# Kernel tuning notes

Hardware: AMD Instinct MI355X
Metric: run time of the kernel (lower is better)

Reference implementation:

```python
import jax, jax.numpy as jnp
import numpy as np

B, T, E, H = 8, 1024, 1024, 16
D = E // H  # per-head dim = 64


def setup_inputs() -> dict:
    key = jax.random.key(0)
    ks = jax.random.split(key, 10)
    s = 0.05
    return {
        "source": jax.random.normal(ks[0], (B, T, E), jnp.float32),
        "target": jax.random.normal(ks[1], (B, T, E), jnp.float32),
        "W_q": jax.random.normal(ks[2], (1, H, D, D), jnp.float32) * s,
        "W_v": jax.random.normal(ks[3], (1, H, D, D), jnp.float32) * s,
        "W_o": jax.random.normal(ks[4], (1, H, D, D), jnp.float32) * s,
        "W_ih": jax.random.normal(ks[5], (H, D, D), jnp.float32) * s,
        "W_hh": jax.random.normal(ks[6], (H, D, D), jnp.float32) * s,
        "b_ih": jax.random.normal(ks[7], (H, D), jnp.float32) * s,
        "b_hh": jax.random.normal(ks[8], (H, D), jnp.float32) * s,
    }


def reference(source, target, W_q, W_v, W_o, W_ih, W_hh, b_ih, b_hh):
    b, t, e = source.shape
    h = W_ih.shape[0]
    d = e // h
    # split heads: [B, H, T, d]
    q = source.reshape(b, t, h, d).transpose(0, 2, 1, 3)
    k = target.reshape(b, t, h, d).transpose(0, 2, 1, 3)
    v = k
    # per-head projections (grammar path: k is NOT projected)
    q = jnp.einsum('bhtd,hde->bhte', q, W_q[0])
    v = jnp.einsum('bhtd,hde->bhte', v, W_v[0])
    # RNN positional key generation (per head, batch_first nn.RNN, tanh).
    # step 0: input = k[:, :, 0, :], hidden = 0  ->  h1 = tanh(x @ Wih^T + b_ih + b_hh)
    k0 = k[:, :, 0, :]  # [B, H, d]
    h1 = jnp.tanh(jnp.einsum('bhd,hed->bhe', k0, W_ih) + b_ih + b_hh)
    # steps t>=1: next_word fed back as BOTH input and hidden state
    def step(hs, _):
        hn = jnp.tanh(jnp.einsum('bhd,hed->bhe', hs, W_ih) + b_ih
                      + jnp.einsum('bhd,hed->bhe', hs, W_hh) + b_hh)
        return hn, hn
    _, rest = jax.lax.scan(step, h1, None, length=t - 1)  # [T-1, B, H, d]
    nw = jnp.concatenate([h1[None], rest], axis=0).transpose(1, 2, 0, 3)  # [B,H,T,d]
    # scores / sqrt(d)  (time_attention), then merge_attn divides by sqrt(T)
    scores = jnp.einsum('bhqd,bhkd->bhqk', q, nw) / float(np.sqrt(d))
    w = jax.nn.softmax(scores / float(np.sqrt(t)), axis=-1)
    out = jnp.einsum('bhqk,bhkd->bhqd', w, v)
    out = jnp.einsum('bhtd,hde->bhte', out, W_o[0])
    return out.transpose(0, 2, 1, 3).reshape(b, t, e)
```

## Files before the change

kernel.cpp:

```cpp
#include <hip/hip_runtime.h>

typedef unsigned short u16;
typedef short short8 __attribute__((ext_vector_type(8)));
typedef float f32x4 __attribute__((ext_vector_type(4)));
typedef _Float16 f16;
typedef f16 f16x2 __attribute__((ext_vector_type(2)));
typedef f16 f16x8 __attribute__((ext_vector_type(8)));

#define B_ 8
#define T_ 1024
#define E_ 1024
#define H_ 16
#define D_ 64
#define BH_ 128

__device__ __forceinline__ float ftanh(float x){
    x = fminf(8.0f, fmaxf(-8.0f, x));
    float e2 = __expf(2.0f * x);
    return 1.0f - 2.0f * __builtin_amdgcn_rcpf(e2 + 1.0f);
}

__device__ __forceinline__ u16 f2h(float x){
    union { f16 h; u16 u; } v; v.h = (f16)x; return v.u;
}

__device__ __forceinline__ float dot8(f16x8 a, f16x8 b, float acc){
#if __has_builtin(__builtin_amdgcn_fdot2)
    f16x2 a0 = {a[0],a[1]}, a1 = {a[2],a[3]}, a2 = {a[4],a[5]}, a3 = {a[6],a[7]};
    f16x2 b0 = {b[0],b[1]}, b1 = {b[2],b[3]}, b2 = {b[4],b[5]}, b3 = {b[6],b[7]};
    acc = __builtin_amdgcn_fdot2(a0, b0, acc, false);
    acc = __builtin_amdgcn_fdot2(a1, b1, acc, false);
    acc = __builtin_amdgcn_fdot2(a2, b2, acc, false);
    acc = __builtin_amdgcn_fdot2(a3, b3, acc, false);
#else
    #pragma unroll
    for (int i = 0; i < 8; ++i) acc += (float)a[i] * (float)b[i];
#endif
    return acc;
}

__device__ __forceinline__ f16x8 pack8(f32x4 a, f32x4 b){
    f16x8 r;
    r[0]=(f16)a[0]; r[1]=(f16)a[1]; r[2]=(f16)a[2]; r[3]=(f16)a[3];
    r[4]=(f16)b[0]; r[5]=(f16)b[1]; r[6]=(f16)b[2]; r[7]=(f16)b[3];
    return r;
}

#define PIN8(x) do { f32x4 _t = __builtin_bit_cast(f32x4, x); \
                     asm volatile("" : "+v"(_t));             \
                     x = __builtin_bit_cast(f16x8, _t); } while (0)

__global__ __launch_bounds__(256, 1) void proj_rnn_kernel(
    const float* __restrict__ src, const float* __restrict__ tgt,
    const float* __restrict__ Wq,  const float* __restrict__ Wv,
    const float* __restrict__ Wih, const float* __restrict__ Whh,
    const float* __restrict__ bih, const float* __restrict__ bhh,
    u16* __restrict__ qh, u16* __restrict__ vh, u16* __restrict__ nwh)
{
    int bid = blockIdx.x;
    if (bid < BH_) {
        if (threadIdx.x >= 64) return;
        __shared__ __align__(16) u16 hl[D_];
        const int b = bid >> 4, h = bid & 15;
        const int e = threadIdx.x;

        const f32x4* wi4 = (const f32x4*)(Wih + ((size_t)h * D_ + e) * D_);
        const f32x4* wh4 = (const f32x4*)(Whh + ((size_t)h * D_ + e) * D_);
        float c = bih[h * D_ + e] + bhh[h * D_ + e];
        asm volatile("" : "+v"(c));

        f16x8 n0 = pack8(wi4[0],  wi4[1]),  n1 = pack8(wi4[2],  wi4[3]);
        f16x8 n2 = pack8(wi4[4],  wi4[5]),  n3 = pack8(wi4[6],  wi4[7]);
        f16x8 n4 = pack8(wi4[8],  wi4[9]),  n5 = pack8(wi4[10], wi4[11]);
        f16x8 n6 = pack8(wi4[12], wi4[13]), n7 = pack8(wi4[14], wi4[15]);
        f16x8 m0 = pack8(wi4[0]+wh4[0],   wi4[1]+wh4[1]);
        f16x8 m1 = pack8(wi4[2]+wh4[2],   wi4[3]+wh4[3]);
        f16x8 m2 = pack8(wi4[4]+wh4[4],   wi4[5]+wh4[5]);
        f16x8 m3 = pack8(wi4[6]+wh4[6],   wi4[7]+wh4[7]);
        f16x8 m4 = pack8(wi4[8]+wh4[8],   wi4[9]+wh4[9]);
        f16x8 m5 = pack8(wi4[10]+wh4[10], wi4[11]+wh4[11]);
        f16x8 m6 = pack8(wi4[12]+wh4[12], wi4[13]+wh4[13]);
        f16x8 m7 = pack8(wi4[14]+wh4[14], wi4[15]+wh4[15]);
        PIN8(m0); PIN8(m1); PIN8(m2); PIN8(m3);
        PIN8(m4); PIN8(m5); PIN8(m6); PIN8(m7);

        hl[e] = f2h(tgt[(size_t)b * T_ * E_ + h * D_ + e]);

        u16* nwp = nwh + (size_t)bid * T_ * D_;
        const f16x8* hl8 = (const f16x8*)hl;

        {
            f16x8 x0=hl8[0],x1=hl8[1],x2=hl8[2],x3=hl8[3],
                  x4=hl8[4],x5=hl8[5],x6=hl8[6],x7=hl8[7];
            float s0=dot8(n0,x0,c),   s1=dot8(n1,x1,0.f),
                  s2=dot8(n2,x2,0.f), s3=dot8(n3,x3,0.f),
                  s4=dot8(n4,x4,0.f), s5=dot8(n5,x5,0.f),
                  s6=dot8(n6,x6,0.f), s7=dot8(n7,x7,0.f);
            float hv = ftanh(((s0+s1)+(s2+s3)) + ((s4+s5)+(s6+s7)));
            u16 hb = f2h(hv);
            hl[e] = hb;
            nwp[e] = hb;
        }

        #pragma unroll 1
        for (int t = 1; t < T_; ++t) {
            f16x8 x0=hl8[0],x1=hl8[1],x2=hl8[2],x3=hl8[3],
                  x4=hl8[4],x5=hl8[5],x6=hl8[6],x7=hl8[7];
            float s0=dot8(m0,x0,c),   s1=dot8(m1,x1,0.f),
                  s2=dot8(m2,x2,0.f), s3=dot8(m3,x3,0.f),
                  s4=dot8(m4,x4,0.f), s5=dot8(m5,x5,0.f),
                  s6=dot8(m6,x6,0.f), s7=dot8(m7,x7,0.f);
            float hv = ftanh(((s0+s1)+(s2+s3)) + ((s4+s5)+(s6+s7)));
            u16 hb = f2h(hv);
            hl[e] = hb;
            nwp[(size_t)t * D_ + e] = hb;
        }
    } else {
        int pb   = bid - BH_;
        int bh   = pb >> 5;
        int tile = pb & 31;
        int b = bh >> 4, h = bh & 15;
        int e  = threadIdx.x & 63;
        int tg = threadIdx.x >> 6;
        int t0 = tile * 32 + tg * 8;

        const float* wq = Wq + (size_t)h * D_ * D_ + e;
        const float* wv = Wv + (size_t)h * D_ * D_ + e;
        const float* s0 = src + ((size_t)b * T_ + t0) * E_ + h * D_;
        const float* g0 = tgt + ((size_t)b * T_ + t0) * E_ + h * D_;

        float aq[8] = {0,0,0,0,0,0,0,0};
        float av[8] = {0,0,0,0,0,0,0,0};
        #pragma unroll 4
        for (int d4 = 0; d4 < 16; ++d4) {
            float q0 = wq[(4*d4+0)*64], q1 = wq[(4*d4+1)*64],
                  q2 = wq[(4*d4+2)*64], q3 = wq[(4*d4+3)*64];
            float v0 = wv[(4*d4+0)*64], v1 = wv[(4*d4+1)*64],
                  v2 = wv[(4*d4+2)*64], v3 = wv[(4*d4+3)*64];
            #pragma unroll
            for (int j = 0; j < 8; ++j) {
                float4 x = *(const float4*)(s0 + (size_t)j * E_ + 4*d4);
                float4 y = *(const float4*)(g0 + (size_t)j * E_ + 4*d4);
                aq[j] += x.x*q0 + x.y*q1 + x.z*q2 + x.w*q3;
                av[j] += y.x*v0 + y.y*v1 + y.z*v2 + y.w*v3;
            }
        }
        u16* qp = qh + ((size_t)bh * T_ + t0) * D_ + e;
        #pragma unroll
        for (int j = 0; j < 8; ++j) qp[(size_t)j * D_] = f2h(aq[j] * (1.0f/256.0f));
        f16x8 vv;
        #pragma unroll
        for (int j = 0; j < 8; ++j) vv[j] = (f16)av[j];
        *(f16x8*)(vh + ((size_t)bh * D_ + e) * T_ + t0) = vv;
    }
}

#define MFMA16(a, b, c) __builtin_amdgcn_mfma_f32_16x16x32_f16(a, b, c, 0, 0, 0)

__global__ __launch_bounds__(256) void attn_kernel(
    const u16* __restrict__ qh,
    const u16* __restrict__ kh,
    const u16* __restrict__ vh,
    const float* __restrict__ Wo,
    float* __restrict__ out)
{
    __shared__ __align__(16) u16 Klds[64 * 64];
    __shared__ __align__(16) u16 Vlds[64 * 64];
    __shared__ __align__(16) u16 Plds[4][16 * 64];

    const int tid  = threadIdx.x;
    const int lane = tid & 63;
    const int w    = tid >> 6;
    const int l15  = lane & 15;
    const int quad = lane >> 4;
    const int sw   = lane & 7;
    const int bh   = blockIdx.y;
    const int qt   = blockIdx.x;

    const size_t base  = (size_t)bh * T_ * D_;
    const size_t vbase = (size_t)bh * D_ * T_;

    f16x8 aq0, aq1;
    {
        int qrow = qt * 64 + w * 16 + l15;
        const f16x8* qp = (const f16x8*)(qh + base + (size_t)qrow * 64 + quad * 8);
        aq0 = qp[0];
        aq1 = qp[4];
    }

    f32x4 oacc[4];
    #pragma unroll
    for (int i = 0; i < 4; ++i) oacc[i] = (f32x4){0.f, 0.f, 0.f, 0.f};
    float lrun[4] = {0.f, 0.f, 0.f, 0.f};

    u16* Pw = Plds[w];

    #pragma unroll 1
    for (int kt = 0; kt < 16; ++kt) {
        #pragma unroll
        for (int i = 0; i < 2; ++i) {
            int ch = tid + 256 * i;
            int r = ch >> 3, cc = ch & 7;
            short8 kval = *(const short8*)(kh + base + (size_t)(kt * 64 + r) * 64 + cc * 8);
            *(short8*)&Klds[r * 64 + ((cc ^ (r & 7)) * 8)] = kval;
            short8 vval = *(const short8*)(vh + vbase + (size_t)r * T_ + kt * 64 + cc * 8);
            *(short8*)&Vlds[r * 64 + ((cc ^ (r & 7)) * 8)] = vval;
        }
        __syncthreads();

        f32x4 sacc[4];
        #pragma unroll
        for (int u = 0; u < 4; ++u) {
            sacc[u] = (f32x4){0.f, 0.f, 0.f, 0.f};
            int row = 16 * u + l15;
            f16x8 bk0 = *(const f16x8*)&Klds[row * 64 + (((quad + 0) ^ sw) * 8)];
            f16x8 bk1 = *(const f16x8*)&Klds[row * 64 + (((quad + 4) ^ sw) * 8)];
            sacc[u] = MFMA16(aq0, bk0, sacc[u]);
            sacc[u] = MFMA16(aq1, bk1, sacc[u]);
        }

        float pr[4][4];
        #pragma unroll
        for (int r = 0; r < 4; ++r) {
            float rs = 0.f;
            #pragma unroll
            for (int u = 0; u < 4; ++u) {
                float pv = __expf(sacc[u][r]);
                pr[u][r] = pv;
                rs += pv;
            }
            #pragma unroll
            for (int off = 1; off < 16; off <<= 1)
                rs += __shfl_xor(rs, off, 16);
            lrun[r] += rs;
        }

        #pragma unroll
        for (int u = 0; u < 4; ++u) {
            int col = 16 * u + l15;
            #pragma unroll
            for (int r = 0; r < 4; ++r) {
                int row = quad * 4 + r;
                Pw[row * 64 + (((col >> 3) ^ (row & 7)) * 8) + (col & 7)] = f2h(pr[u][r]);
            }
        }

        #pragma unroll
        for (int kc = 0; kc < 2; ++kc) {
            f16x8 ap = *(const f16x8*)&Pw[l15 * 64 + (((quad + 4 * kc) ^ sw) * 8)];
            #pragma unroll
            for (int nt = 0; nt < 4; ++nt) {
                int drow = 16 * nt + l15;
                f16x8 bv = *(const f16x8*)&Vlds[drow * 64 + (((quad + 4 * kc) ^ sw) * 8)];
                oacc[nt] = MFMA16(ap, bv, oacc[nt]);
            }
        }
        __syncthreads();
    }

    const int b  = bh >> 4, hh = bh & 15;
    {
        const float* wo = Wo + (size_t)hh * D_ * D_;
        #pragma unroll
        for (int i = 0; i < 2; ++i) {
            int ch = tid + 256 * i;
            int e = ch >> 3, dc = ch & 7;
            short8 vch;
            #pragma unroll
            for (int j = 0; j < 8; ++j)
                vch[j] = (short)f2h(wo[(size_t)(dc * 8 + j) * D_ + e]);
            *(short8*)&Klds[e * 64 + ((dc ^ (e & 7)) * 8)] = vch;
        }
    }
    #pragma unroll
    for (int nt = 0; nt < 4; ++nt) {
        int col = 16 * nt + l15;
        #pragma unroll
        for (int r = 0; r < 4; ++r) {
            int row = quad * 4 + r;
            Pw[row * 64 + (((col >> 3) ^ (row & 7)) * 8) + (col & 7)] =
                f2h(oacc[nt][r] / lrun[r]);
        }
    }
    __syncthreads();

    f16x8 ao0 = *(const f16x8*)&Pw[l15 * 64 + (((quad + 0) ^ sw) * 8)];
    f16x8 ao1 = *(const f16x8*)&Pw[l15 * 64 + (((quad + 4) ^ sw) * 8)];
    f32x4 oo[4];
    #pragma unroll
    for (int nt = 0; nt < 4; ++nt) {
        oo[nt] = (f32x4){0.f, 0.f, 0.f, 0.f};
        int erow = 16 * nt + l15;
        f16x8 b0 = *(const f16x8*)&Klds[erow * 64 + (((quad + 0) ^ (erow & 7)) * 8)];
        f16x8 b1 = *(const f16x8*)&Klds[erow * 64 + (((quad + 4) ^ (erow & 7)) * 8)];
        oo[nt] = MFMA16(ao0, b0, oo[nt]);
        oo[nt] = MFMA16(ao1, b1, oo[nt]);
    }
    #pragma unroll
    for (int nt = 0; nt < 4; ++nt) {
        #pragma unroll
        for (int r = 0; r < 4; ++r) {
            int qg = qt * 64 + w * 16 + quad * 4 + r;
            int e  = 16 * nt + l15;
            out[((size_t)b * T_ + qg) * E_ + hh * D_ + e] = oo[nt][r];
        }
    }
}

extern "C" void kernel_launch(void* const* d_in, const int* in_sizes, int n_in,
                              void* d_out, int out_size, void* d_ws, size_t ws_size,
                              hipStream_t stream)
{
    const float* src = (const float*)d_in[0];
    const float* tgt = (const float*)d_in[1];
    const float* Wq  = (const float*)d_in[2];
    const float* Wv  = (const float*)d_in[3];
    const float* Wo  = (const float*)d_in[4];
    const float* Wih = (const float*)d_in[5];
    const float* Whh = (const float*)d_in[6];
    const float* bih = (const float*)d_in[7];
    const float* bhh = (const float*)d_in[8];
    float* out = (float*)d_out;

    char* ws = (char*)d_ws;
    u16* qh  = (u16*)(ws);
    u16* vh  = (u16*)(ws + (size_t)16 * 1024 * 1024);
    u16* nwh = (u16*)(ws + (size_t)32 * 1024 * 1024);

    (void)in_sizes; (void)n_in; (void)out_size; (void)ws_size;

    proj_rnn_kernel<<<dim3(BH_ + 4096), 256, 0, stream>>>(
        src, tgt, Wq, Wv, Wih, Whh, bih, bhh, qh, vh, nwh);
    attn_kernel<<<dim3(16, BH_), 256, 0, stream>>>(qh, nwh, vh, Wo, out);
}
```

Measured before the change: 398.8 us.

## Replace LDS-based RNN hidden-state exchange with DPP and permlane register gathers

The serial RNN recurrence previously wrote each step's hidden value to shared memory and read back all 64 values per lane. Now each lane handles one output across 4 row-partials: it gathers 16 neighbouring halves via DPP row permutes, computes 4 partial dot products, and reduces across 16- and 32-lane groups with permlane swaps, falling back to shuffles if the swap semantics don't match. The weights are pre-permuted to match the gather order. This removes LDS round-trip latency from the critical sequential path, at the cost of more cross-lane ops and a more intricate lane mapping.

```diff
diff --git a/kernel.cpp b/kernel.cpp
--- a/kernel.cpp
+++ b/kernel.cpp
@@ -1,6 +1,7 @@
 #include <hip/hip_runtime.h>
 
 typedef unsigned short u16;
+typedef unsigned int   u32;
 typedef short short8 __attribute__((ext_vector_type(8)));
 typedef float f32x4 __attribute__((ext_vector_type(4)));
 typedef _Float16 f16;
@@ -24,31 +25,83 @@
     union { f16 h; u16 u; } v; v.h = (f16)x; return v.u;
 }
 
-__device__ __forceinline__ float dot8(f16x8 a, f16x8 b, float acc){
-#if __has_builtin(__builtin_amdgcn_fdot2)
-    f16x2 a0 = {a[0],a[1]}, a1 = {a[2],a[3]}, a2 = {a[4],a[5]}, a3 = {a[6],a[7]};
-    f16x2 b0 = {b[0],b[1]}, b1 = {b[2],b[3]}, b2 = {b[4],b[5]}, b3 = {b[6],b[7]};
-    acc = __builtin_amdgcn_fdot2(a0, b0, acc, false);
-    acc = __builtin_amdgcn_fdot2(a1, b1, acc, false);
-    acc = __builtin_amdgcn_fdot2(a2, b2, acc, false);
-    acc = __builtin_amdgcn_fdot2(a3, b3, acc, false);
-#else
-    #pragma unroll
-    for (int i = 0; i < 8; ++i) acc += (float)a[i] * (float)b[i];
-#endif
-    return acc;
-}
-
-__device__ __forceinline__ f16x8 pack8(f32x4 a, f32x4 b){
-    f16x8 r;
-    r[0]=(f16)a[0]; r[1]=(f16)a[1]; r[2]=(f16)a[2]; r[3]=(f16)a[3];
-    r[4]=(f16)b[0]; r[5]=(f16)b[1]; r[6]=(f16)b[2]; r[7]=(f16)b[3];
-    return r;
-}
-
-#define PIN8(x) do { f32x4 _t = __builtin_bit_cast(f32x4, x); \
-                     asm volatile("" : "+v"(_t));             \
-                     x = __builtin_bit_cast(f16x8, _t); } while (0)
+__device__ __forceinline__ float h2f(u16 u){
+    union { u16 u; f16 h; } v; v.u = u; return (float)v.h;
+}
+
+#define DPPC(s, ctrl) ((u32)__builtin_amdgcn_update_dpp(0, (int)(s), (ctrl), 0xF, 0xF, false))
+
+struct G8 { u32 r0, r1, r2, r3, r4, r5, r6, r7; };
+
+__device__ __forceinline__ G8 gather16(u32 a){
+    G8 g;
+    u32 t = DPPC(a, 0xB1);
+    g.r0 = a | (t << 16);
+    g.r1 = DPPC(g.r0, 0x4E);
+    g.r2 = DPPC(g.r0, 0x124);
+    g.r3 = DPPC(g.r1, 0x124);
+    g.r4 = DPPC(g.r0, 0x128);
+    g.r5 = DPPC(g.r1, 0x128);
+    g.r6 = DPPC(g.r2, 0x128);
+    g.r7 = DPPC(g.r3, 0x128);
+    return g;
+}
+
+__device__ __forceinline__ float fd(u32 w, u32 x, float acc){
+    return __builtin_amdgcn_fdot2(__builtin_bit_cast(f16x2, w),
+                                  __builtin_bit_cast(f16x2, x), acc, false);
+}
+
+__device__ __forceinline__ float perm16x(float v, bool sel){
+    u32 a = __builtin_bit_cast(u32, v), b = a;
+    asm volatile("v_permlane16_swap_b32 %0, %1" : "+v"(a), "+v"(b));
+    return __builtin_bit_cast(float, sel ? a : b);
+}
+__device__ __forceinline__ float perm32x(float v, bool sel){
+    u32 a = __builtin_bit_cast(u32, v), b = a;
+    asm volatile("v_permlane32_swap_b32 %0, %1" : "+v"(a), "+v"(b));
+    return __builtin_bit_cast(float, sel ? a : b);
+}
+
+template<bool USEPERM>
+__device__ __forceinline__ u32 rnn_step(u32 hbits, const u32 (&W)[4][8], float cbias,
+                                        bool q1f, bool q2f, bool sel16, bool sel32)
+{
+    G8 g = gather16(hbits);
+    float p0 = fd(W[0][0], g.r0, 0.f);
+    float p1 = fd(W[1][0], g.r0, 0.f);
+    float p2 = fd(W[2][0], g.r0, 0.f);
+    float p3 = fd(W[3][0], g.r0, 0.f);
+    p0 = fd(W[0][1], g.r1, p0); p1 = fd(W[1][1], g.r1, p1);
+    p2 = fd(W[2][1], g.r1, p2); p3 = fd(W[3][1], g.r1, p3);
+    p0 = fd(W[0][2], g.r2, p0); p1 = fd(W[1][2], g.r2, p1);
+    p2 = fd(W[2][2], g.r2, p2); p3 = fd(W[3][2], g.r2, p3);
+    p0 = fd(W[0][3], g.r3, p0); p1 = fd(W[1][3], g.r3, p1);
+    p2 = fd(W[2][3], g.r3, p2); p3 = fd(W[3][3], g.r3, p3);
+    p0 = fd(W[0][4], g.r4, p0); p1 = fd(W[1][4], g.r4, p1);
+    p2 = fd(W[2][4], g.r4, p2); p3 = fd(W[3][4], g.r4, p3);
+    p0 = fd(W[0][5], g.r5, p0); p1 = fd(W[1][5], g.r5, p1);
+    p2 = fd(W[2][5], g.r5, p2); p3 = fd(W[3][5], g.r5, p3);
+    p0 = fd(W[0][6], g.r6, p0); p1 = fd(W[1][6], g.r6, p1);
+    p2 = fd(W[2][6], g.r6, p2); p3 = fd(W[3][6], g.r6, p3);
+    p0 = fd(W[0][7], g.r7, p0); p1 = fd(W[1][7], g.r7, p1);
+    p2 = fd(W[2][7], g.r7, p2); p3 = fd(W[3][7], g.r7, p3);
+
+    float A0 = q1f ? p1 : p0, S0 = q1f ? p0 : p1;
+    float A1 = q1f ? p3 : p2, S1 = q1f ? p2 : p3;
+    if (USEPERM) {
+        A0 += perm16x(S0, sel16);
+        A1 += perm16x(S1, sel16);
+    } else {
+        A0 += __shfl_xor(S0, 16);
+        A1 += __shfl_xor(S1, 16);
+    }
+    float K  = q2f ? A1 : A0;
+    float SS = q2f ? A0 : A1;
+    float recv = USEPERM ? perm32x(SS, sel32) : __shfl_xor(SS, 32);
+    float yv = K + recv;
+    return (u32)f2h(ftanh(yv + cbias));
+}
 
 __global__ __launch_bounds__(256, 1) void proj_rnn_kernel(
     const float* __restrict__ src, const float* __restrict__ tgt,
@@ -60,60 +113,74 @@
     int bid = blockIdx.x;
     if (bid < BH_) {
         if (threadIdx.x >= 64) return;
-        __shared__ __align__(16) u16 hl[D_];
         const int b = bid >> 4, h = bid & 15;
-        const int e = threadIdx.x;
-
-        const f32x4* wi4 = (const f32x4*)(Wih + ((size_t)h * D_ + e) * D_);
-        const f32x4* wh4 = (const f32x4*)(Whh + ((size_t)h * D_ + e) * D_);
-        float c = bih[h * D_ + e] + bhh[h * D_ + e];
-        asm volatile("" : "+v"(c));
-
-        f16x8 n0 = pack8(wi4[0],  wi4[1]),  n1 = pack8(wi4[2],  wi4[3]);
-        f16x8 n2 = pack8(wi4[4],  wi4[5]),  n3 = pack8(wi4[6],  wi4[7]);
-        f16x8 n4 = pack8(wi4[8],  wi4[9]),  n5 = pack8(wi4[10], wi4[11]);
-        f16x8 n6 = pack8(wi4[12], wi4[13]), n7 = pack8(wi4[14], wi4[15]);
-        f16x8 m0 = pack8(wi4[0]+wh4[0],   wi4[1]+wh4[1]);
-        f16x8 m1 = pack8(wi4[2]+wh4[2],   wi4[3]+wh4[3]);
-        f16x8 m2 = pack8(wi4[4]+wh4[4],   wi4[5]+wh4[5]);
-        f16x8 m3 = pack8(wi4[6]+wh4[6],   wi4[7]+wh4[7]);
-        f16x8 m4 = pack8(wi4[8]+wh4[8],   wi4[9]+wh4[9]);
-        f16x8 m5 = pack8(wi4[10]+wh4[10], wi4[11]+wh4[11]);
-        f16x8 m6 = pack8(wi4[12]+wh4[12], wi4[13]+wh4[13]);
-        f16x8 m7 = pack8(wi4[14]+wh4[14], wi4[15]+wh4[15]);
-        PIN8(m0); PIN8(m1); PIN8(m2); PIN8(m3);
-        PIN8(m4); PIN8(m5); PIN8(m6); PIN8(m7);
-
-        hl[e] = f2h(tgt[(size_t)b * T_ * E_ + h * D_ + e]);
+        const int l = threadIdx.x;
+        const bool q1f = (l & 16) != 0;
+        const bool q2f = (l & 32) != 0;
+
+        G8 cg = gather16((u32)f2h((float)l));
+        int kidx[16];
+        kidx[0]  = (int)h2f((u16)(cg.r0 & 0xFFFF)); kidx[1]  = (int)h2f((u16)(cg.r0 >> 16));
+        kidx[2]  = (int)h2f((u16)(cg.r1 & 0xFFFF)); kidx[3]  = (int)h2f((u16)(cg.r1 >> 16));
+        kidx[4]  = (int)h2f((u16)(cg.r2 & 0xFFFF)); kidx[5]  = (int)h2f((u16)(cg.r2 >> 16));
+        kidx[6]  = (int)h2f((u16)(cg.r3 & 0xFFFF)); kidx[7]  = (int)h2f((u16)(cg.r3 >> 16));
+        kidx[8]  = (int)h2f((u16)(cg.r4 & 0xFFFF)); kidx[9]  = (int)h2f((u16)(cg.r4 >> 16));
+        kidx[10] = (int)h2f((u16)(cg.r5 & 0xFFFF)); kidx[11] = (int)h2f((u16)(cg.r5 >> 16));
+        kidx[12] = (int)h2f((u16)(cg.r6 & 0xFFFF)); kidx[13] = (int)h2f((u16)(cg.r6 >> 16));
+        kidx[14] = (int)h2f((u16)(cg.r7 & 0xFFFF)); kidx[15] = (int)h2f((u16)(cg.r7 >> 16));
+
+        u32 sx = (u32)l, sy = (u32)l;
+        asm volatile("v_permlane16_swap_b32 %0, %1" : "+v"(sx), "+v"(sy));
+        const bool sel16 = (sx == (u32)(l ^ 16));
+        const bool ok16  = sel16 || (sy == (u32)(l ^ 16));
+        u32 tx = (u32)l, ty = (u32)l;
+        asm volatile("v_permlane32_swap_b32 %0, %1" : "+v"(tx), "+v"(ty));
+        const bool sel32 = (tx == (u32)(l ^ 32));
+        const bool ok32  = sel32 || (ty == (u32)(l ^ 32));
+
+        const float* WI = Wih + (size_t)h * D_ * D_;
+        const float* WH = Whh + (size_t)h * D_ * D_;
+        float cbias = bih[h * D_ + l] + bhh[h * D_ + l];
+        u32 wm[4][8], wn[4][8];
+        #pragma unroll
+        for (int i = 0; i < 4; ++i) {
+            const float* wiR = WI + (size_t)((l & 15) + 16 * i) * D_;
+            const float* whR = WH + (size_t)((l & 15) + 16 * i) * D_;
+            #pragma unroll
+            for (int j = 0; j < 8; ++j) {
+                int k0 = kidx[2 * j], k1 = kidx[2 * j + 1];
+                float wI0 = wiR[k0], wI1 = wiR[k1];
+                float wH0 = whR[k0], wH1 = whR[k1];
+                wn[i][j] = (u32)f2h(wI0)       | ((u32)f2h(wI1)       << 16);
+                wm[i][j] = (u32)f2h(wI0 + wH0) | ((u32)f2h(wI1 + wH1) << 16);
+            }
+        }
+        #pragma unroll
+        for (int i = 0; i < 4; ++i)
+            #pragma unroll
+            for (int j = 0; j < 8; ++j)
+                asm volatile("" : "+v"(wm[i][j]));
+        asm volatile("" : "+v"(cbias));
 
         u16* nwp = nwh + (size_t)bid * T_ * D_;
-        const f16x8* hl8 = (const f16x8*)hl;
-
-        {
-            f16x8 x0=hl8[0],x1=hl8[1],x2=hl8[2],x3=hl8[3],
-                  x4=hl8[4],x5=hl8[5],x6=hl8[6],x7=hl8[7];
-            float s0=dot8(n0,x0,c),   s1=dot8(n1,x1,0.f),
-                  s2=dot8(n2,x2,0.f), s3=dot8(n3,x3,0.f),
-                  s4=dot8(n4,x4,0.f), s5=dot8(n5,x5,0.f),
-                  s6=dot8(n6,x6,0.f), s7=dot8(n7,x7,0.f);
-            float hv = ftanh(((s0+s1)+(s2+s3)) + ((s4+s5)+(s6+s7)));
-            u16 hb = f2h(hv);
-            hl[e] = hb;
-            nwp[e] = hb;
-        }
-
-        #pragma unroll 1
-        for (int t = 1; t < T_; ++t) {
-            f16x8 x0=hl8[0],x1=hl8[1],x2=hl8[2],x3=hl8[3],
-                  x4=hl8[4],x5=hl8[5],x6=hl8[6],x7=hl8[7];
-            float s0=dot8(m0,x0,c),   s1=dot8(m1,x1,0.f),
-                  s2=dot8(m2,x2,0.f), s3=dot8(m3,x3,0.f),
-                  s4=dot8(m4,x4,0.f), s5=dot8(m5,x5,0.f),
-                  s6=dot8(m6,x6,0.f), s7=dot8(m7,x7,0.f);
-            float hv = ftanh(((s0+s1)+(s2+s3)) + ((s4+s5)+(s6+s7)));
-            u16 hb = f2h(hv);
-            hl[e] = hb;
-            nwp[(size_t)t * D_ + e] = hb;
+        u32 hb = (u32)f2h(tgt[(size_t)b * T_ * E_ + h * D_ + l]);
+
+        if (__all(ok16 && ok32)) {
+            hb = rnn_step<true>(hb, wn, cbias, q1f, q2f, sel16, sel32);
+            nwp[l] = (u16)hb;
+            #pragma unroll 1
+            for (int t = 1; t < T_; ++t) {
+                hb = rnn_step<true>(hb, wm, cbias, q1f, q2f, sel16, sel32);
+                nwp[(size_t)t * D_ + l] = (u16)hb;
+            }
+        } else {
+            hb = rnn_step<false>(hb, wn, cbias, q1f, q2f, sel16, sel32);
+            nwp[l] = (u16)hb;
+            #pragma unroll 1
+            for (int t = 1; t < T_; ++t) {
+                hb = rnn_step<false>(hb, wm, cbias, q1f, q2f, sel16, sel32);
+                nwp[(size_t)t * D_ + l] = (u16)hb;
+            }
         }
     } else {
         int pb   = bid - BH_;
```

Result: slower. 417.1 us (+4.6%).

## Process two query tiles per warp to reuse K/V LDS tiles

Applied to the files above, without the earlier changes.

Each block now handles 128 query rows instead of 64, with each warp computing two 16-row groups against the same K and V tiles loaded into LDS. This halves the grid and the number of times K/V are fetched from global memory and staged. The per-row softmax sum reduction across lanes is deferred from every key tile to the end, and the division becomes a reciprocal multiply. It raises register use and LDS for P, and halves the block count, which lowers parallelism (1024 blocks).

```diff
diff --git a/kernel.cpp b/kernel.cpp
--- a/kernel.cpp
+++ b/kernel.cpp
@@ -166,7 +166,7 @@
 {
     __shared__ __align__(16) u16 Klds[64 * 64];
     __shared__ __align__(16) u16 Vlds[64 * 64];
-    __shared__ __align__(16) u16 Plds[4][16 * 64];
+    __shared__ __align__(16) u16 Plds[4][2][16 * 64];
 
     const int tid  = threadIdx.x;
     const int lane = tid & 63;
@@ -180,20 +180,24 @@
     const size_t base  = (size_t)bh * T_ * D_;
     const size_t vbase = (size_t)bh * D_ * T_;
 
-    f16x8 aq0, aq1;
-    {
-        int qrow = qt * 64 + w * 16 + l15;
+    f16x8 aq[2][2];
+    #pragma unroll
+    for (int g = 0; g < 2; ++g) {
+        int qrow = qt * 128 + (w + 4 * g) * 16 + l15;
         const f16x8* qp = (const f16x8*)(qh + base + (size_t)qrow * 64 + quad * 8);
-        aq0 = qp[0];
-        aq1 = qp[4];
-    }
-
-    f32x4 oacc[4];
-    #pragma unroll
-    for (int i = 0; i < 4; ++i) oacc[i] = (f32x4){0.f, 0.f, 0.f, 0.f};
-    float lrun[4] = {0.f, 0.f, 0.f, 0.f};
-
-    u16* Pw = Plds[w];
+        aq[g][0] = qp[0];
+        aq[g][1] = qp[4];
+    }
+
+    f32x4 oacc[2][4];
+    float lrun[2][4];
+    #pragma unroll
+    for (int g = 0; g < 2; ++g)
+        #pragma unroll
+        for (int i = 0; i < 4; ++i) {
+            oacc[g][i] = (f32x4){0.f, 0.f, 0.f, 0.f};
+            lrun[g][i] = 0.f;
+        }
 
     #pragma unroll 1
     for (int kt = 0; kt < 16; ++kt) {
@@ -208,55 +212,73 @@
         }
         __syncthreads();
 
-        f32x4 sacc[4];
+        f32x4 sacc[2][4];
         #pragma unroll
         for (int u = 0; u < 4; ++u) {
-            sacc[u] = (f32x4){0.f, 0.f, 0.f, 0.f};
             int row = 16 * u + l15;
             f16x8 bk0 = *(const f16x8*)&Klds[row * 64 + (((quad + 0) ^ sw) * 8)];
             f16x8 bk1 = *(const f16x8*)&Klds[row * 64 + (((quad + 4) ^ sw) * 8)];
-            sacc[u] = MFMA16(aq0, bk0, sacc[u]);
-            sacc[u] = MFMA16(aq1, bk1, sacc[u]);
-        }
-
-        float pr[4][4];
+            #pragma unroll
+            for (int g = 0; g < 2; ++g) {
+                f32x4 z = (f32x4){0.f, 0.f, 0.f, 0.f};
+                z = MFMA16(aq[g][0], bk0, z);
+                z = MFMA16(aq[g][1], bk1, z);
+                sacc[g][u] = z;
+            }
+        }
+
+        #pragma unroll
+        for (int g = 0; g < 2; ++g) {
+            float pr[4][4];
+            #pragma unroll
+            for (int r = 0; r < 4; ++r) {
+                float rs = 0.f;
+                #pragma unroll
+                for (int u = 0; u < 4; ++u) {
+                    float pv = __expf(sacc[g][u][r]);
+                    pr[u][r] = pv;
+                    rs += pv;
+                }
+                lrun[g][r] += rs;
+            }
+            u16* Pw = Plds[w][g];
+            #pragma unroll
+            for (int u = 0; u < 4; ++u) {
+                int col = 16 * u + l15;
+                #pragma unroll
+                for (int r = 0; r < 4; ++r) {
+                    int row = quad * 4 + r;
+                    Pw[row * 64 + (((col >> 3) ^ (row & 7)) * 8) + (col & 7)] = f2h(pr[u][r]);
+                }
+            }
+        }
+
+        #pragma unroll
+        for (int kc = 0; kc < 2; ++kc) {
+            int csel = ((quad + 4 * kc) ^ sw) * 8;
+            f16x8 ap0 = *(const f16x8*)&Plds[w][0][l15 * 64 + csel];
+            f16x8 ap1 = *(const f16x8*)&Plds[w][1][l15 * 64 + csel];
+            #pragma unroll
+            for (int nt = 0; nt < 4; ++nt) {
+                f16x8 bv = *(const f16x8*)&Vlds[(16 * nt + l15) * 64 + csel];
+                oacc[0][nt] = MFMA16(ap0, bv, oacc[0][nt]);
+                oacc[1][nt] = MFMA16(ap1, bv, oacc[1][nt]);
+            }
+        }
+        __syncthreads();
+    }
+
+    float inv[2][4];
+    #pragma unroll
+    for (int g = 0; g < 2; ++g)
         #pragma unroll
         for (int r = 0; r < 4; ++r) {
-            float rs = 0.f;
-            #pragma unroll
-            for (int u = 0; u < 4; ++u) {
-                float pv = __expf(sacc[u][r]);
-                pr[u][r] = pv;
-                rs += pv;
-            }
+            float s = lrun[g][r];
             #pragma unroll
             for (int off = 1; off < 16; off <<= 1)
-                rs += __shfl_xor(rs, off, 16);
-            lrun[r] += rs;
-        }
-
-        #pragma unroll
-        for (int u = 0; u < 4; ++u) {
-            int col = 16 * u + l15;
-            #pragma unroll
-            for (int r = 0; r < 4; ++r) {
-                int row = quad * 4 + r;
-                Pw[row * 64 + (((col >> 3) ^ (row & 7)) * 8) + (col & 7)] = f2h(pr[u][r]);
-            }
-        }
-
-        #pragma unroll
-        for (int kc = 0; kc < 2; ++kc) {
-            f16x8 ap = *(const f16x8*)&Pw[l15 * 64 + (((quad + 4 * kc) ^ sw) * 8)];
-            #pragma unroll
-            for (int nt = 0; nt < 4; ++nt) {
-                int drow = 16 * nt + l15;
-                f16x8 bv = *(const f16x8*)&Vlds[drow * 64 + (((quad + 4 * kc) ^ sw) * 8)];
-                oacc[nt] = MFMA16(ap, bv, oacc[nt]);
-            }
-        }
-        __syncthreads();
-    }
+                s += __shfl_xor(s, off, 16);
+            inv[g][r] = __builtin_amdgcn_rcpf(s);
+        }
 
     const int b  = bh >> 4, hh = bh & 15;
     {
@@ -273,38 +295,54 @@
         }
     }
     #pragma unroll
+    for (int g = 0; g < 2; ++g) {
+        u16* Pw = Plds[w][g];
+        #pragma unroll
+        for (int nt = 0; nt < 4; ++nt) {
+            int col = 16 * nt + l15;
+            #pragma unroll
+            for (int r = 0; r < 4; ++r) {
+                int row = quad * 4 + r;
+                Pw[row * 64 + (((col >> 3) ^ (row & 7)) * 8) + (col & 7)] =
+                    f2h(oacc[g][nt][r] * inv[g][r]);
+            }
+        }
+    }
+    __syncthreads();
+
+    f16x8 ao[2][2];
+    #pragma unroll
+    for (int g = 0; g < 2; ++g) {
+        ao[g][0] = *(const f16x8*)&Plds[w][g][l15 * 64 + (((quad + 0) ^ sw) * 8)];
+        ao[g][1] = *(const f16x8*)&Plds[w][g][l15 * 64 + (((quad + 4) ^ sw) * 8)];
+    }
+    f32x4 oo[2][4];
+    #pragma unroll
+    for (int g = 0; g < 2; ++g)
+        #pragma unroll
+        for (int nt = 0; nt < 4; ++nt)
+            oo[g][nt] = (f32x4){0.f, 0.f, 0.f, 0.f};
+    #pragma unroll
     for (int nt = 0; nt < 4; ++nt) {
-        int col = 16 * nt + l15;
-        #pragma unroll
-        for (int r = 0; r < 4; ++r) {
-            int row = quad * 4 + r;
-            Pw[row * 64 + (((col >> 3) ^ (row & 7)) * 8) + (col & 7)] =
-                f2h(oacc[nt][r] / lrun[r]);
-        }
-    }
-    __syncthreads();
-
-    f16x8 ao0 = *(const f16x8*)&Pw[l15 * 64 + (((quad + 0) ^ sw) * 8)];
-    f16x8 ao1 = *(const f16x8*)&Pw[l15 * 64 + (((quad + 4) ^ sw) * 8)];
-    f32x4 oo[4];
-    #pragma unroll
-    for (int nt = 0; nt < 4; ++nt) {
-        oo[nt] = (f32x4){0.f, 0.f, 0.f, 0.f};
         int erow = 16 * nt + l15;
         f16x8 b0 = *(const f16x8*)&Klds[erow * 64 + (((quad + 0) ^ (erow & 7)) * 8)];
         f16x8 b1 = *(const f16x8*)&Klds[erow * 64 + (((quad + 4) ^ (erow & 7)) * 8)];
-        oo[nt] = MFMA16(ao0, b0, oo[nt]);
-        oo[nt] = MFMA16(ao1, b1, oo[nt]);
-    }
-    #pragma unroll
-    for (int nt = 0; nt < 4; ++nt) {
-        #pragma unroll
-        for (int r = 0; r < 4; ++r) {
-            int qg = qt * 64 + w * 16 + quad * 4 + r;
-            int e  = 16 * nt + l15;
-            out[((size_t)b * T_ + qg) * E_ + hh * D_ + e] = oo[nt][r];
-        }
-    }
+        #pragma unroll
+        for (int g = 0; g < 2; ++g) {
+            oo[g][nt] = MFMA16(ao[g][0], b0, oo[g][nt]);
+            oo[g][nt] = MFMA16(ao[g][1], b1, oo[g][nt]);
+        }
+    }
+    #pragma unroll
+    for (int g = 0; g < 2; ++g)
+        #pragma unroll
+        for (int nt = 0; nt < 4; ++nt)
+            #pragma unroll
+            for (int r = 0; r < 4; ++r) {
+                int qg = qt * 128 + (w + 4 * g) * 16 + quad * 4 + r;
+                int e  = 16 * nt + l15;
+                out[((size_t)b * T_ + qg) * E_ + hh * D_ + e] = oo[g][nt][r];
+            }
 }
 
 extern "C" void kernel_launch(void* const* d_in, const int* in_sizes, int n_in,
@@ -331,5 +369,5 @@
 
     proj_rnn_kernel<<<dim3(BH_ + 4096), 256, 0, stream>>>(
         src, tgt, Wq, Wv, Wih, Whh, bih, bhh, qh, vh, nwh);
-    attn_kernel<<<dim3(16, BH_), 256, 0, stream>>>(qh, nwh, vh, Wo, out);
-}
+    attn_kernel<<<dim3(8, BH_), 256, 0, stream>>>(qh, nwh, vh, Wo, out);
+}
```

Measured after the change: 374.5 us. 6.1% less time.
